# Kernel tuning notes

Measured on AMD Instinct MI355X. Metric: run time of the kernel, lower is better.

Reference implementation:

```python
import jax, jax.numpy as jnp
import numpy as np

EPS = 1e-5
N, K, C = 32768, 27, 128


def setup_inputs() -> dict:
    key = jax.random.key(0)
    k1, k2, k3, k4 = jax.random.split(key, 4)
    feats = jax.random.normal(k1, (N, C), dtype=jnp.float32)
    # Precomputed kernel-offset neighbor map (MinkowskiEngine kernel map),
    # one input index per (point, kernel offset).
    neighbors = jax.random.randint(k2, (N, K), 0, N, dtype=jnp.int32)
    scale = 1.0 / np.sqrt(K * C)  # fan-in init like sparse conv
    W1 = jax.random.normal(k3, (K, C, C), dtype=jnp.float32) * scale
    W2 = jax.random.normal(k4, (K, C, C), dtype=jnp.float32) * scale
    g1 = jnp.ones((C,), jnp.float32)
    b1 = jnp.zeros((C,), jnp.float32)
    g2 = jnp.ones((C,), jnp.float32)
    b2 = jnp.zeros((C,), jnp.float32)
    return {"feats": feats, "neighbors": neighbors, "W1": W1, "g1": g1,
            "b1": b1, "W2": W2, "g2": g2, "b2": b2}


def _sparse_conv(f, nbr, W):
    # gather-GEMM-scatter: gather neighbor features per kernel offset,
    # contract with that offset's weight, sum over offsets.
    gathered = f[nbr]                      # [N, K, C]
    return jnp.einsum('nkc,kcd->nd', gathered, W)  # [N, C]


def _batch_norm(x, gamma, beta):
    mu = jnp.mean(x, axis=0)
    var = jnp.mean(jnp.square(x - mu), axis=0)
    return (x - mu) * jax.lax.rsqrt(var + EPS) * gamma + beta


def reference(feats, neighbors, W1, g1, b1, W2, g2, b2):
    out = _sparse_conv(feats, neighbors, W1)
    out = jax.nn.relu(_batch_norm(out, g1, b1))
    out = _sparse_conv(out, neighbors, W2)
    out = _batch_norm(out, g2, b2)
    return jax.nn.relu(out + feats)
```

## Files before the change

### kernel.cpp

```cpp
#include <hip/hip_runtime.h>
#include <stdint.h>

#define NPTS 32768
#define KOFF 27
#define CH   128
#define NC   (NPTS*CH)
#define KSPLIT 3
#define KPG  9
#define TILE_M 128
#define NITER (KPG*2)

typedef __attribute__((ext_vector_type(8))) short short8;
typedef __attribute__((ext_vector_type(4))) float f32x4;
typedef unsigned short u16;

__device__ __forceinline__ float bf2f(u16 u) {
    union { uint32_t i; float f; } v; v.i = ((uint32_t)u) << 16; return v.f;
}
__device__ __forceinline__ u16 f2bf(float f) {
    union { float f; uint32_t i; } v; v.f = f;
    return (u16)((v.i + 0x7FFF + ((v.i >> 16) & 1)) >> 16);
}

#define GLDS16(gp, lp) __builtin_amdgcn_global_load_lds( \
    (__attribute__((address_space(1))) void*)(gp),           \
    (__attribute__((address_space(3))) void*)(lp), 16, 0, 0)

__global__ __launch_bounds__(256)
void prep_kernel(const float* __restrict__ W1, const float* __restrict__ W2,
                 u16* __restrict__ W1t, u16* __restrict__ W2t,
                 const float* __restrict__ feats, u16* __restrict__ xbuf,
                 float* __restrict__ stat)
{
    __shared__ u16 t[128*129];
    const int b = blockIdx.x, tid = threadIdx.x;
    if (b < 2*KOFF) {
        if (b == 0) for (int i = tid; i < 512; i += 256) stat[i] = 0.0f;
        const float* src = (b < KOFF) ? W1 + (size_t)b*CH*CH : W2 + (size_t)(b-KOFF)*CH*CH;
        u16* dst         = (b < KOFF) ? W1t + (size_t)b*CH*CH : W2t + (size_t)(b-KOFF)*CH*CH;
        for (int e = tid; e < CH*CH; e += 256) {
            int c = e >> 7, d = e & 127;
            t[d*129 + c] = f2bf(src[e]);
        }
        __syncthreads();
        for (int e = tid; e < CH*CH; e += 256) {
            int d = e >> 7, c = e & 127;
            dst[e] = t[d*129 + c];
        }
    } else {
        size_t e = ((size_t)(b - 2*KOFF) * 256 + tid) * 8;
        float4 a = *(const float4*)(feats + e);
        float4 c = *(const float4*)(feats + e + 4);
        ushort4 lo, hi;
        lo.x = f2bf(a.x); lo.y = f2bf(a.y); lo.z = f2bf(a.z); lo.w = f2bf(a.w);
        hi.x = f2bf(c.x); hi.y = f2bf(c.y); hi.z = f2bf(c.z); hi.w = f2bf(c.w);
        *(ushort4*)(xbuf + e) = lo;
        *(ushort4*)(xbuf + e + 4) = hi;
    }
}

__global__ __launch_bounds__(256, 3)
void ResidualBlock_77498389889548_kernel(const u16* __restrict__ xb,
                                         const int* __restrict__ nbr,
                                         const u16* __restrict__ Wt,
                                         u16* __restrict__ part)
{
    __shared__ __align__(16) u16 A_lds[TILE_M*64];
    __shared__ __align__(16) u16 B_lds[CH*64];
    __shared__ int idx_lds[KPG*TILE_M];

    const int tid = threadIdx.x;
    const int n0  = blockIdx.x * TILE_M;
    const int kg  = blockIdx.y;

    for (int e = tid; e < KPG*TILE_M; e += 256) {
        int kk = e >> 7, r = e & 127;
        int nb = nbr[(size_t)(n0 + r)*KOFF + kg*KPG + kk];
        idx_lds[e] = ((unsigned)nb < (unsigned)NPTS) ? nb : 0;
    }
    __syncthreads();

    const int wave = tid >> 6;
    const int lane = tid & 63;
    const int wrow = (wave >> 1) * 64;
    const int wcol = (wave & 1) * 64;
    const int lm   = lane & 15;
    const int quad = lane >> 4;
    const int l8r  = lane >> 3;
    const int swz  = ((lane & 7) ^ l8r) << 3;

    f32x4 acc[4][4];
    #pragma unroll
    for (int i = 0; i < 4; ++i)
        #pragma unroll
        for (int j = 0; j < 4; ++j)
            #pragma unroll
            for (int r = 0; r < 4; ++r) acc[i][j][r] = 0.0f;

    int aoff[2][4], boff[2][4];
    #pragma unroll
    for (int kc = 0; kc < 2; ++kc) {
        int g = kc*4 + quad;
        #pragma unroll
        for (int i = 0; i < 4; ++i) {
            int row = wrow + i*16 + lm;
            aoff[kc][i] = row*128 + ((g ^ (row & 7)) << 4);
        }
        #pragma unroll
        for (int j = 0; j < 4; ++j) {
            int d = wcol + j*16 + lm;
            boff[kc][j] = d*128 + ((g ^ (d & 7)) << 4);
        }
    }

    const char* Ab = (const char*)A_lds;
    const char* Bb = (const char*)B_lds;

    for (int it = 0; it < NITER; ++it) {
        const int h  = (it >= KPG) ? 1 : 0;
        const int kk = it - h*KPG;

        const u16* wb = Wt + (size_t)(kg*KPG + kk)*CH*CH + h*64 + swz;
        #pragma unroll
        for (int j = 0; j < 4; ++j) {
            int row8 = wave*32 + j*8;
            GLDS16(wb + (size_t)(row8 + l8r)*CH, &B_lds[row8*64]);
        }
        int nb4[4];
        #pragma unroll
        for (int j = 0; j < 4; ++j)
            nb4[j] = idx_lds[kk*128 + wave*32 + j*8 + l8r];
        #pragma unroll
        for (int j = 0; j < 4; ++j) {
            int row8 = wave*32 + j*8;
            GLDS16(xb + (size_t)nb4[j]*CH + h*64 + swz, &A_lds[row8*64]);
        }
        __syncthreads();

        #pragma unroll
        for (int kc = 0; kc < 2; ++kc) {
            short8 a[4], b[4];
            #pragma unroll
            for (int i = 0; i < 4; ++i) a[i] = *(const short8*)(Ab + aoff[kc][i]);
            #pragma unroll
            for (int j = 0; j < 4; ++j) b[j] = *(const short8*)(Bb + boff[kc][j]);
            #pragma unroll
            for (int i = 0; i < 4; ++i)
                #pragma unroll
                for (int j = 0; j < 4; ++j)
                    acc[i][j] = __builtin_amdgcn_mfma_f32_16x16x32_bf16(a[i], b[j], acc[i][j], 0, 0, 0);
        }
        __syncthreads();
    }

    u16* pb = part + (size_t)kg * NC;
    const int colb = wcol + lm;
    #pragma unroll
    for (int i = 0; i < 4; ++i) {
        #pragma unroll
        for (int r = 0; r < 4; ++r) {
            int row = n0 + wrow + i*16 + quad*4 + r;
            u16* pp = pb + (size_t)row*CH + colb;
            #pragma unroll
            for (int j = 0; j < 4; ++j) pp[j*16] = f2bf(acc[i][j][r]);
        }
    }
}

__global__ __launch_bounds__(256)
void sumstats_kernel(const u16* __restrict__ p0, const u16* __restrict__ p1,
                     const u16* __restrict__ p2, u16* __restrict__ y,
                     float* __restrict__ gsum, float* __restrict__ gsq)
{
    __shared__ float ls[CH], lq[CH];
    const int tid = threadIdx.x;
    const int c8 = (tid & 15) * 8;
    const int r0 = tid >> 4;
    const int b = blockIdx.x;
    if (tid < CH) { ls[tid] = 0.0f; lq[tid] = 0.0f; }
    __syncthreads();

    float s[8], q[8];
    #pragma unroll
    for (int i = 0; i < 8; ++i) { s[i] = 0.0f; q[i] = 0.0f; }

    for (int r = r0; r < 128; r += 16) {
        size_t e = (size_t)(b*128 + r)*CH + c8;
        ushort4 a0 = *(const ushort4*)(p0 + e), a1 = *(const ushort4*)(p0 + e + 4);
        ushort4 b0 = *(const ushort4*)(p1 + e), b1 = *(const ushort4*)(p1 + e + 4);
        ushort4 d0 = *(const ushort4*)(p2 + e), d1 = *(const ushort4*)(p2 + e + 4);
        float v[8];
        v[0] = bf2f(a0.x) + bf2f(b0.x) + bf2f(d0.x);
        v[1] = bf2f(a0.y) + bf2f(b0.y) + bf2f(d0.y);
        v[2] = bf2f(a0.z) + bf2f(b0.z) + bf2f(d0.z);
        v[3] = bf2f(a0.w) + bf2f(b0.w) + bf2f(d0.w);
        v[4] = bf2f(a1.x) + bf2f(b1.x) + bf2f(d1.x);
        v[5] = bf2f(a1.y) + bf2f(b1.y) + bf2f(d1.y);
        v[6] = bf2f(a1.z) + bf2f(b1.z) + bf2f(d1.z);
        v[7] = bf2f(a1.w) + bf2f(b1.w) + bf2f(d1.w);
        ushort4 o0, o1;
        o0.x = f2bf(v[0]); o0.y = f2bf(v[1]); o0.z = f2bf(v[2]); o0.w = f2bf(v[3]);
        o1.x = f2bf(v[4]); o1.y = f2bf(v[5]); o1.z = f2bf(v[6]); o1.w = f2bf(v[7]);
        *(ushort4*)(y + e) = o0;
        *(ushort4*)(y + e + 4) = o1;
        #pragma unroll
        for (int i = 0; i < 8; ++i) { s[i] += v[i]; q[i] += v[i]*v[i]; }
    }
    #pragma unroll
    for (int i = 0; i < 8; ++i) {
        atomicAdd(&ls[c8 + i], s[i]);
        atomicAdd(&lq[c8 + i], q[i]);
    }
    __syncthreads();
    if (tid < CH) {
        atomicAdd(&gsum[tid], ls[tid]);
        atomicAdd(&gsq[tid],  lq[tid]);
    }
}

__global__ __launch_bounds__(256)
void norm_relu_kernel(const u16* __restrict__ y, const float* __restrict__ sums,
                      const float* __restrict__ sumsq, const float* __restrict__ gam,
                      const float* __restrict__ bet, u16* __restrict__ xo)
{
    __shared__ float sc[128], sh[128];
    const int tid = threadIdx.x;
    if (tid < 128) {
        float mu  = sums[tid] * (1.0f/NPTS);
        float var = fmaxf(sumsq[tid] * (1.0f/NPTS) - mu*mu, 0.0f);
        float rs  = rsqrtf(var + 1e-5f);
        float s   = rs * gam[tid];
        sc[tid] = s; sh[tid] = bet[tid] - mu*s;
    }
    __syncthreads();
    size_t e = ((size_t)blockIdx.x*256 + tid) * 8;
    int c0 = (int)(e & 127);
    ushort4 lo = *(const ushort4*)(y + e);
    ushort4 hi = *(const ushort4*)(y + e + 4);
    ushort4 o0, o1;
    o0.x = f2bf(fmaxf(bf2f(lo.x)*sc[c0+0] + sh[c0+0], 0.0f));
    o0.y = f2bf(fmaxf(bf2f(lo.y)*sc[c0+1] + sh[c0+1], 0.0f));
    o0.z = f2bf(fmaxf(bf2f(lo.z)*sc[c0+2] + sh[c0+2], 0.0f));
    o0.w = f2bf(fmaxf(bf2f(lo.w)*sc[c0+3] + sh[c0+3], 0.0f));
    o1.x = f2bf(fmaxf(bf2f(hi.x)*sc[c0+4] + sh[c0+4], 0.0f));
    o1.y = f2bf(fmaxf(bf2f(hi.y)*sc[c0+5] + sh[c0+5], 0.0f));
    o1.z = f2bf(fmaxf(bf2f(hi.z)*sc[c0+6] + sh[c0+6], 0.0f));
    o1.w = f2bf(fmaxf(bf2f(hi.w)*sc[c0+7] + sh[c0+7], 0.0f));
    *(ushort4*)(xo + e) = o0;
    *(ushort4*)(xo + e + 4) = o1;
}

__global__ __launch_bounds__(256)
void final_kernel(const u16* __restrict__ y, const float* __restrict__ sums,
                  const float* __restrict__ sumsq, const float* __restrict__ gam,
                  const float* __restrict__ bet, const float* __restrict__ feats,
                  float* __restrict__ out)
{
    __shared__ float sc[128], sh[128];
    const int tid = threadIdx.x;
    if (tid < 128) {
        float mu  = sums[tid] * (1.0f/NPTS);
        float var = fmaxf(sumsq[tid] * (1.0f/NPTS) - mu*mu, 0.0f);
        float rs  = rsqrtf(var + 1e-5f);
        float s   = rs * gam[tid];
        sc[tid] = s; sh[tid] = bet[tid] - mu*s;
    }
    __syncthreads();
    size_t e = ((size_t)blockIdx.x*256 + tid) * 4;
    int c0 = (int)(e & 127);
    ushort4 in = *(const ushort4*)(y + e);
    float4 ft = *(const float4*)(feats + e);
    float4 o;
    o.x = fmaxf(bf2f(in.x)*sc[c0+0] + sh[c0+0] + ft.x, 0.0f);
    o.y = fmaxf(bf2f(in.y)*sc[c0+1] + sh[c0+1] + ft.y, 0.0f);
    o.z = fmaxf(bf2f(in.z)*sc[c0+2] + sh[c0+2] + ft.z, 0.0f);
    o.w = fmaxf(bf2f(in.w)*sc[c0+3] + sh[c0+3] + ft.w, 0.0f);
    *(float4*)(out + e) = o;
}

extern "C" void kernel_launch(void* const* d_in, const int* in_sizes, int n_in,
                              void* d_out, int out_size, void* d_ws, size_t ws_size,
                              hipStream_t stream)
{
    const float* feats = (const float*)d_in[0];
    const int*   nbr   = (const int*)d_in[1];
    const float* W1    = (const float*)d_in[2];
    const float* g1    = (const float*)d_in[3];
    const float* b1    = (const float*)d_in[4];
    const float* W2    = (const float*)d_in[5];
    const float* g2    = (const float*)d_in[6];
    const float* b2    = (const float*)d_in[7];
    float* out = (float*)d_out;

    char* ws = (char*)d_ws;
    u16*   xbuf = (u16*)ws;
    u16*   prt  = xbuf + (size_t)NC;
    u16*   ybuf = prt + (size_t)3*NC;
    u16*   W1t  = ybuf + (size_t)NC;
    u16*   W2t  = W1t + (size_t)KOFF*CH*CH;
    float* stat = (float*)(W2t + (size_t)KOFF*CH*CH);

    prep_kernel<<<dim3(2*KOFF + NC/2048), 256, 0, stream>>>(W1, W2, W1t, W2t, feats, xbuf, stat);

    ResidualBlock_77498389889548_kernel<<<dim3(NPTS/TILE_M, KSPLIT), 256, 0, stream>>>(
        xbuf, nbr, W1t, prt);
    sumstats_kernel<<<dim3(NPTS/128), 256, 0, stream>>>(
        prt, prt + (size_t)NC, prt + (size_t)2*NC, ybuf, stat, stat + 128);
    norm_relu_kernel<<<dim3(NC/2048), 256, 0, stream>>>(ybuf, stat, stat + 128, g1, b1, xbuf);

    ResidualBlock_77498389889548_kernel<<<dim3(NPTS/TILE_M, KSPLIT), 256, 0, stream>>>(
        xbuf, nbr, W2t, prt);
    sumstats_kernel<<<dim3(NPTS/128), 256, 0, stream>>>(
        prt, prt + (size_t)NC, prt + (size_t)2*NC, ybuf, stat + 256, stat + 384);
    final_kernel<<<dim3(NC/1024), 256, 0, stream>>>(ybuf, stat + 256, stat + 384, g2, b2, feats, out);
}
```

Before: 197.1 us.

## Drop K-split, double-buffer LDS tiles, fuse batch-norm stats into conv epilogue

The conv kernel now handles all 27 kernel offsets per 128-row tile instead of splitting them across three blocks. This removes the three bf16 partial buffers and the separate sumstats pass. The gather/weight loads go through double-buffered LDS, so the next stage's global-to-LDS copy overlaps the current MFMA work. The epilogue writes bf16 outputs directly and accumulates per-channel sum and sum-of-squares into global stats via atomics. The grid shrinks to 256 blocks with launch bounds of 1 block per CU and twice the LDS, which reduces occupancy and parallelism. Statistics are now computed from fp32 accumulators rather than from rounded partial sums.

```diff
diff --git a/kernel.cpp b/kernel.cpp
--- a/kernel.cpp
+++ b/kernel.cpp
@@ -5,10 +5,8 @@
 #define KOFF 27
 #define CH   128
 #define NC   (NPTS*CH)
-#define KSPLIT 3
-#define KPG  9
 #define TILE_M 128
-#define NITER (KPG*2)
+#define NITER (KOFF*2)
 
 typedef __attribute__((ext_vector_type(8))) short short8;
 typedef __attribute__((ext_vector_type(4))) float f32x4;
@@ -59,25 +57,28 @@
     }
 }
 
-__global__ __launch_bounds__(256, 3)
+__global__ __launch_bounds__(256, 1)
 void ResidualBlock_77498389889548_kernel(const u16* __restrict__ xb,
                                          const int* __restrict__ nbr,
                                          const u16* __restrict__ Wt,
-                                         u16* __restrict__ part)
-{
-    __shared__ __align__(16) u16 A_lds[TILE_M*64];
-    __shared__ __align__(16) u16 B_lds[CH*64];
-    __shared__ int idx_lds[KPG*TILE_M];
+                                         u16* __restrict__ y,
+                                         float* __restrict__ gsum,
+                                         float* __restrict__ gsq)
+{
+    __shared__ __align__(16) u16 A_lds[2][TILE_M*64];
+    __shared__ __align__(16) u16 B_lds[2][CH*64];
+    __shared__ int idx_lds[KOFF*TILE_M];
+    __shared__ float ls[CH], lq[CH];
 
     const int tid = threadIdx.x;
     const int n0  = blockIdx.x * TILE_M;
-    const int kg  = blockIdx.y;
-
-    for (int e = tid; e < KPG*TILE_M; e += 256) {
-        int kk = e >> 7, r = e & 127;
-        int nb = nbr[(size_t)(n0 + r)*KOFF + kg*KPG + kk];
-        idx_lds[e] = ((unsigned)nb < (unsigned)NPTS) ? nb : 0;
-    }
+
+    const int* nbl = nbr + (size_t)n0 * KOFF;
+    for (int e = tid; e < KOFF*TILE_M; e += 256) {
+        int v = nbl[e];
+        idx_lds[e] = ((unsigned)v < (unsigned)NPTS) ? v : 0;
+    }
+    if (tid < CH) { ls[tid] = 0.0f; lq[tid] = 0.0f; }
     __syncthreads();
 
     const int wave = tid >> 6;
@@ -113,30 +114,37 @@
         }
     }
 
-    const char* Ab = (const char*)A_lds;
-    const char* Bb = (const char*)B_lds;
-
+    #define STAGE(buf, it)                                                     \
+    {                                                                          \
+        const int h_  = ((it) >= KOFF) ? 1 : 0;                                \
+        const int kk_ = (it) - h_*KOFF;                                        \
+        const u16* wb_ = Wt + (size_t)kk_*CH*CH + h_*64 + swz;                 \
+        _Pragma("unroll")                                                      \
+        for (int j_ = 0; j_ < 4; ++j_) {                                       \
+            int row8_ = wave*32 + j_*8;                                        \
+            GLDS16(wb_ + (size_t)(row8_ + l8r)*CH, &B_lds[buf][row8_*64]);     \
+        }                                                                      \
+        int nb4_[4];                                                           \
+        _Pragma("unroll")                                                      \
+        for (int j_ = 0; j_ < 4; ++j_)                                         \
+            nb4_[j_] = idx_lds[(wave*32 + j_*8 + l8r)*KOFF + kk_];             \
+        _Pragma("unroll")                                                      \
+        for (int j_ = 0; j_ < 4; ++j_) {                                       \
+            int row8_ = wave*32 + j_*8;                                        \
+            GLDS16(xb + (size_t)nb4_[j_]*CH + h_*64 + swz,                     \
+                   &A_lds[buf][row8_*64]);                                     \
+        }                                                                      \
+    }
+
+    STAGE(0, 0);
+    __syncthreads();
+
+    int cur = 0;
     for (int it = 0; it < NITER; ++it) {
-        const int h  = (it >= KPG) ? 1 : 0;
-        const int kk = it - h*KPG;
-
-        const u16* wb = Wt + (size_t)(kg*KPG + kk)*CH*CH + h*64 + swz;
-        #pragma unroll
-        for (int j = 0; j < 4; ++j) {
-            int row8 = wave*32 + j*8;
-            GLDS16(wb + (size_t)(row8 + l8r)*CH, &B_lds[row8*64]);
-        }
-        int nb4[4];
-        #pragma unroll
-        for (int j = 0; j < 4; ++j)
-            nb4[j] = idx_lds[kk*128 + wave*32 + j*8 + l8r];
-        #pragma unroll
-        for (int j = 0; j < 4; ++j) {
-            int row8 = wave*32 + j*8;
-            GLDS16(xb + (size_t)nb4[j]*CH + h*64 + swz, &A_lds[row8*64]);
-        }
-        __syncthreads();
-
+        if (it + 1 < NITER) STAGE(cur ^ 1, it + 1);
+
+        const char* Ab = (const char*)A_lds[cur];
+        const char* Bb = (const char*)B_lds[cur];
         #pragma unroll
         for (int kc = 0; kc < 2; ++kc) {
             short8 a[4], b[4];
@@ -151,65 +159,31 @@
                     acc[i][j] = __builtin_amdgcn_mfma_f32_16x16x32_bf16(a[i], b[j], acc[i][j], 0, 0, 0);
         }
         __syncthreads();
-    }
-
-    u16* pb = part + (size_t)kg * NC;
-    const int colb = wcol + lm;
+        cur ^= 1;
+    }
+    #undef STAGE
+
+    float s[4], q[4];
+    #pragma unroll
+    for (int j = 0; j < 4; ++j) { s[j] = 0.0f; q[j] = 0.0f; }
     #pragma unroll
     for (int i = 0; i < 4; ++i) {
         #pragma unroll
         for (int r = 0; r < 4; ++r) {
             int row = n0 + wrow + i*16 + quad*4 + r;
-            u16* pp = pb + (size_t)row*CH + colb;
-            #pragma unroll
-            for (int j = 0; j < 4; ++j) pp[j*16] = f2bf(acc[i][j][r]);
-        }
-    }
-}
-
-__global__ __launch_bounds__(256)
-void sumstats_kernel(const u16* __restrict__ p0, const u16* __restrict__ p1,
-                     const u16* __restrict__ p2, u16* __restrict__ y,
-                     float* __restrict__ gsum, float* __restrict__ gsq)
-{
-    __shared__ float ls[CH], lq[CH];
-    const int tid = threadIdx.x;
-    const int c8 = (tid & 15) * 8;
-    const int r0 = tid >> 4;
-    const int b = blockIdx.x;
-    if (tid < CH) { ls[tid] = 0.0f; lq[tid] = 0.0f; }
-    __syncthreads();
-
-    float s[8], q[8];
-    #pragma unroll
-    for (int i = 0; i < 8; ++i) { s[i] = 0.0f; q[i] = 0.0f; }
-
-    for (int r = r0; r < 128; r += 16) {
-        size_t e = (size_t)(b*128 + r)*CH + c8;
-        ushort4 a0 = *(const ushort4*)(p0 + e), a1 = *(const ushort4*)(p0 + e + 4);
-        ushort4 b0 = *(const ushort4*)(p1 + e), b1 = *(const ushort4*)(p1 + e + 4);
-        ushort4 d0 = *(const ushort4*)(p2 + e), d1 = *(const ushort4*)(p2 + e + 4);
-        float v[8];
-        v[0] = bf2f(a0.x) + bf2f(b0.x) + bf2f(d0.x);
-        v[1] = bf2f(a0.y) + bf2f(b0.y) + bf2f(d0.y);
-        v[2] = bf2f(a0.z) + bf2f(b0.z) + bf2f(d0.z);
-        v[3] = bf2f(a0.w) + bf2f(b0.w) + bf2f(d0.w);
-        v[4] = bf2f(a1.x) + bf2f(b1.x) + bf2f(d1.x);
-        v[5] = bf2f(a1.y) + bf2f(b1.y) + bf2f(d1.y);
-        v[6] = bf2f(a1.z) + bf2f(b1.z) + bf2f(d1.z);
-        v[7] = bf2f(a1.w) + bf2f(b1.w) + bf2f(d1.w);
-        ushort4 o0, o1;
-        o0.x = f2bf(v[0]); o0.y = f2bf(v[1]); o0.z = f2bf(v[2]); o0.w = f2bf(v[3]);
-        o1.x = f2bf(v[4]); o1.y = f2bf(v[5]); o1.z = f2bf(v[6]); o1.w = f2bf(v[7]);
-        *(ushort4*)(y + e) = o0;
-        *(ushort4*)(y + e + 4) = o1;
-        #pragma unroll
-        for (int i = 0; i < 8; ++i) { s[i] += v[i]; q[i] += v[i]*v[i]; }
-    }
-    #pragma unroll
-    for (int i = 0; i < 8; ++i) {
-        atomicAdd(&ls[c8 + i], s[i]);
-        atomicAdd(&lq[c8 + i], q[i]);
+            u16* pp = y + (size_t)row*CH + wcol + lm;
+            #pragma unroll
+            for (int j = 0; j < 4; ++j) {
+                float v = acc[i][j][r];
+                pp[j*16] = f2bf(v);
+                s[j] += v; q[j] += v*v;
+            }
+        }
+    }
+    #pragma unroll
+    for (int j = 0; j < 4; ++j) {
+        atomicAdd(&ls[wcol + j*16 + lm], s[j]);
+        atomicAdd(&lq[wcol + j*16 + lm], q[j]);
     }
     __syncthreads();
     if (tid < CH) {
@@ -294,23 +268,18 @@
 
     char* ws = (char*)d_ws;
     u16*   xbuf = (u16*)ws;
-    u16*   prt  = xbuf + (size_t)NC;
-    u16*   ybuf = prt + (size_t)3*NC;
+    u16*   ybuf = xbuf + (size_t)NC;
     u16*   W1t  = ybuf + (size_t)NC;
     u16*   W2t  = W1t + (size_t)KOFF*CH*CH;
     float* stat = (float*)(W2t + (size_t)KOFF*CH*CH);
 
     prep_kernel<<<dim3(2*KOFF + NC/2048), 256, 0, stream>>>(W1, W2, W1t, W2t, feats, xbuf, stat);
 
-    ResidualBlock_77498389889548_kernel<<<dim3(NPTS/TILE_M, KSPLIT), 256, 0, stream>>>(
-        xbuf, nbr, W1t, prt);
-    sumstats_kernel<<<dim3(NPTS/128), 256, 0, stream>>>(
-        prt, prt + (size_t)NC, prt + (size_t)2*NC, ybuf, stat, stat + 128);
+    ResidualBlock_77498389889548_kernel<<<dim3(NPTS/TILE_M), 256, 0, stream>>>(
+        xbuf, nbr, W1t, ybuf, stat, stat + 128);
     norm_relu_kernel<<<dim3(NC/2048), 256, 0, stream>>>(ybuf, stat, stat + 128, g1, b1, xbuf);
 
-    ResidualBlock_77498389889548_kernel<<<dim3(NPTS/TILE_M, KSPLIT), 256, 0, stream>>>(
-        xbuf, nbr, W2t, prt);
-    sumstats_kernel<<<dim3(NPTS/128), 256, 0, stream>>>(
-        prt, prt + (size_t)NC, prt + (size_t)2*NC, ybuf, stat + 256, stat + 384);
+    ResidualBlock_77498389889548_kernel<<<dim3(NPTS/TILE_M), 256, 0, stream>>>(
+        xbuf, nbr, W2t, ybuf, stat + 256, stat + 384);
     final_kernel<<<dim3(NC/1024), 256, 0, stream>>>(ybuf, stat + 256, stat + 384, g2, b2, feats, out);
 }
```

Result: slower. 275.4 us (+39.7%).

## Fuse split-K reduction and BN stats into conv kernel via last-block counter

Applied to the files above, without the earlier changes.

Removes the separate sumstats kernel by having the last of the three K-split blocks for each row tile (detected with a per-tile atomic counter and threadfences) sum the bf16 partials, write y, and accumulate BN sums. This saves two kernel launches and lets the reduction overlap with other GEMM blocks still running. The cost is extra shared memory, a fence and an atomic in every block, plus counters that are zeroed only once per call by prep.

```diff
diff --git a/kernel.cpp b/kernel.cpp
--- a/kernel.cpp
+++ b/kernel.cpp
@@ -35,7 +35,7 @@
     __shared__ u16 t[128*129];
     const int b = blockIdx.x, tid = threadIdx.x;
     if (b < 2*KOFF) {
-        if (b == 0) for (int i = tid; i < 512; i += 256) stat[i] = 0.0f;
+        if (b == 0) for (int i = tid; i < 1024; i += 256) stat[i] = 0.0f;
         const float* src = (b < KOFF) ? W1 + (size_t)b*CH*CH : W2 + (size_t)(b-KOFF)*CH*CH;
         u16* dst         = (b < KOFF) ? W1t + (size_t)b*CH*CH : W2t + (size_t)(b-KOFF)*CH*CH;
         for (int e = tid; e < CH*CH; e += 256) {
@@ -63,11 +63,17 @@
 void ResidualBlock_77498389889548_kernel(const u16* __restrict__ xb,
                                          const int* __restrict__ nbr,
                                          const u16* __restrict__ Wt,
-                                         u16* __restrict__ part)
+                                         u16* __restrict__ part,
+                                         u16* __restrict__ y,
+                                         float* __restrict__ gsum,
+                                         float* __restrict__ gsq,
+                                         int* __restrict__ cnt)
 {
     __shared__ __align__(16) u16 A_lds[TILE_M*64];
     __shared__ __align__(16) u16 B_lds[CH*64];
     __shared__ int idx_lds[KPG*TILE_M];
+    __shared__ float ls[CH], lq[CH];
+    __shared__ int s_old;
 
     const int tid = threadIdx.x;
     const int n0  = blockIdx.x * TILE_M;
@@ -165,56 +171,57 @@
             for (int j = 0; j < 4; ++j) pp[j*16] = f2bf(acc[i][j][r]);
         }
     }
-}
-
-__global__ __launch_bounds__(256)
-void sumstats_kernel(const u16* __restrict__ p0, const u16* __restrict__ p1,
-                     const u16* __restrict__ p2, u16* __restrict__ y,
-                     float* __restrict__ gsum, float* __restrict__ gsq)
-{
-    __shared__ float ls[CH], lq[CH];
-    const int tid = threadIdx.x;
-    const int c8 = (tid & 15) * 8;
-    const int r0 = tid >> 4;
-    const int b = blockIdx.x;
-    if (tid < CH) { ls[tid] = 0.0f; lq[tid] = 0.0f; }
-    __syncthreads();
-
-    float s[8], q[8];
-    #pragma unroll
-    for (int i = 0; i < 8; ++i) { s[i] = 0.0f; q[i] = 0.0f; }
-
-    for (int r = r0; r < 128; r += 16) {
-        size_t e = (size_t)(b*128 + r)*CH + c8;
-        ushort4 a0 = *(const ushort4*)(p0 + e), a1 = *(const ushort4*)(p0 + e + 4);
-        ushort4 b0 = *(const ushort4*)(p1 + e), b1 = *(const ushort4*)(p1 + e + 4);
-        ushort4 d0 = *(const ushort4*)(p2 + e), d1 = *(const ushort4*)(p2 + e + 4);
-        float v[8];
-        v[0] = bf2f(a0.x) + bf2f(b0.x) + bf2f(d0.x);
-        v[1] = bf2f(a0.y) + bf2f(b0.y) + bf2f(d0.y);
-        v[2] = bf2f(a0.z) + bf2f(b0.z) + bf2f(d0.z);
-        v[3] = bf2f(a0.w) + bf2f(b0.w) + bf2f(d0.w);
-        v[4] = bf2f(a1.x) + bf2f(b1.x) + bf2f(d1.x);
-        v[5] = bf2f(a1.y) + bf2f(b1.y) + bf2f(d1.y);
-        v[6] = bf2f(a1.z) + bf2f(b1.z) + bf2f(d1.z);
-        v[7] = bf2f(a1.w) + bf2f(b1.w) + bf2f(d1.w);
-        ushort4 o0, o1;
-        o0.x = f2bf(v[0]); o0.y = f2bf(v[1]); o0.z = f2bf(v[2]); o0.w = f2bf(v[3]);
-        o1.x = f2bf(v[4]); o1.y = f2bf(v[5]); o1.z = f2bf(v[6]); o1.w = f2bf(v[7]);
-        *(ushort4*)(y + e) = o0;
-        *(ushort4*)(y + e + 4) = o1;
-        #pragma unroll
-        for (int i = 0; i < 8; ++i) { s[i] += v[i]; q[i] += v[i]*v[i]; }
-    }
-    #pragma unroll
-    for (int i = 0; i < 8; ++i) {
-        atomicAdd(&ls[c8 + i], s[i]);
-        atomicAdd(&lq[c8 + i], q[i]);
-    }
-    __syncthreads();
-    if (tid < CH) {
-        atomicAdd(&gsum[tid], ls[tid]);
-        atomicAdd(&gsq[tid],  lq[tid]);
+
+    __threadfence();
+    __syncthreads();
+    if (tid == 0) s_old = atomicAdd(&cnt[blockIdx.x], 1);
+    __syncthreads();
+    if (s_old == 2) {
+        __threadfence();
+        if (tid < CH) { ls[tid] = 0.0f; lq[tid] = 0.0f; }
+        __syncthreads();
+
+        const u16* p0 = part;
+        const u16* p1 = part + (size_t)NC;
+        const u16* p2 = part + (size_t)2*NC;
+        const int c8 = (tid & 15) * 8;
+        const int r0 = tid >> 4;
+        float s[8], q[8];
+        #pragma unroll
+        for (int i = 0; i < 8; ++i) { s[i] = 0.0f; q[i] = 0.0f; }
+
+        for (int r = r0; r < TILE_M; r += 16) {
+            size_t e = (size_t)(n0 + r)*CH + c8;
+            ushort4 a0 = *(const ushort4*)(p0 + e), a1 = *(const ushort4*)(p0 + e + 4);
+            ushort4 b0 = *(const ushort4*)(p1 + e), b1 = *(const ushort4*)(p1 + e + 4);
+            ushort4 d0 = *(const ushort4*)(p2 + e), d1 = *(const ushort4*)(p2 + e + 4);
+            float v[8];
+            v[0] = bf2f(a0.x) + bf2f(b0.x) + bf2f(d0.x);
+            v[1] = bf2f(a0.y) + bf2f(b0.y) + bf2f(d0.y);
+            v[2] = bf2f(a0.z) + bf2f(b0.z) + bf2f(d0.z);
+            v[3] = bf2f(a0.w) + bf2f(b0.w) + bf2f(d0.w);
+            v[4] = bf2f(a1.x) + bf2f(b1.x) + bf2f(d1.x);
+            v[5] = bf2f(a1.y) + bf2f(b1.y) + bf2f(d1.y);
+            v[6] = bf2f(a1.z) + bf2f(b1.z) + bf2f(d1.z);
+            v[7] = bf2f(a1.w) + bf2f(b1.w) + bf2f(d1.w);
+            ushort4 o0, o1;
+            o0.x = f2bf(v[0]); o0.y = f2bf(v[1]); o0.z = f2bf(v[2]); o0.w = f2bf(v[3]);
+            o1.x = f2bf(v[4]); o1.y = f2bf(v[5]); o1.z = f2bf(v[6]); o1.w = f2bf(v[7]);
+            *(ushort4*)(y + e) = o0;
+            *(ushort4*)(y + e + 4) = o1;
+            #pragma unroll
+            for (int i = 0; i < 8; ++i) { s[i] += v[i]; q[i] += v[i]*v[i]; }
+        }
+        #pragma unroll
+        for (int i = 0; i < 8; ++i) {
+            atomicAdd(&ls[c8 + i], s[i]);
+            atomicAdd(&lq[c8 + i], q[i]);
+        }
+        __syncthreads();
+        if (tid < CH) {
+            atomicAdd(&gsum[tid], ls[tid]);
+            atomicAdd(&gsq[tid],  lq[tid]);
+        }
     }
 }
 
@@ -299,18 +306,15 @@
     u16*   W1t  = ybuf + (size_t)NC;
     u16*   W2t  = W1t + (size_t)KOFF*CH*CH;
     float* stat = (float*)(W2t + (size_t)KOFF*CH*CH);
+    int*   cnt  = (int*)(stat + 512);
 
     prep_kernel<<<dim3(2*KOFF + NC/2048), 256, 0, stream>>>(W1, W2, W1t, W2t, feats, xbuf, stat);
 
     ResidualBlock_77498389889548_kernel<<<dim3(NPTS/TILE_M, KSPLIT), 256, 0, stream>>>(
-        xbuf, nbr, W1t, prt);
-    sumstats_kernel<<<dim3(NPTS/128), 256, 0, stream>>>(
-        prt, prt + (size_t)NC, prt + (size_t)2*NC, ybuf, stat, stat + 128);
+        xbuf, nbr, W1t, prt, ybuf, stat, stat + 128, cnt);
     norm_relu_kernel<<<dim3(NC/2048), 256, 0, stream>>>(ybuf, stat, stat + 128, g1, b1, xbuf);
 
     ResidualBlock_77498389889548_kernel<<<dim3(NPTS/TILE_M, KSPLIT), 256, 0, stream>>>(
-        xbuf, nbr, W2t, prt);
-    sumstats_kernel<<<dim3(NPTS/128), 256, 0, stream>>>(
-        prt, prt + (size_t)NC, prt + (size_t)2*NC, ybuf, stat + 256, stat + 384);
+        xbuf, nbr, W2t, prt, ybuf, stat + 256, stat + 384, cnt + 256);
     final_kernel<<<dim3(NC/1024), 256, 0, stream>>>(ybuf, stat + 256, stat + 384, g2, b2, feats, out);
 }
```

Result: slower. 445.6 us (+126.1%).

## Fuse BN stats and normalize via in-kernel grid barrier, keeping sums in registers

Applied to the files above, without the earlier changes.

Merges the partial-sum/statistics kernel with the normalize+ReLU (and final residual) kernel. Each block keeps its 128x128 tile of summed values in registers across a software grid barrier (atomic counter plus flag spin). This removes the intermediate bf16 y buffer write and read and one launch per BN. The barrier relies on all 256 blocks being co-resident and adds spin-wait latency. The counters are zeroed in the prep kernel.

```diff
diff --git a/kernel.cpp b/kernel.cpp
--- a/kernel.cpp
+++ b/kernel.cpp
@@ -35,7 +35,7 @@
     __shared__ u16 t[128*129];
     const int b = blockIdx.x, tid = threadIdx.x;
     if (b < 2*KOFF) {
-        if (b == 0) for (int i = tid; i < 512; i += 256) stat[i] = 0.0f;
+        if (b == 0) for (int i = tid; i < 1024; i += 256) stat[i] = 0.0f;
         const float* src = (b < KOFF) ? W1 + (size_t)b*CH*CH : W2 + (size_t)(b-KOFF)*CH*CH;
         u16* dst         = (b < KOFF) ? W1t + (size_t)b*CH*CH : W2t + (size_t)(b-KOFF)*CH*CH;
         for (int e = tid; e < CH*CH; e += 256) {
@@ -167,44 +167,60 @@
     }
 }
 
+__device__ __forceinline__ void grid_barrier(int* cnt, int nblk)
+{
+    __threadfence();
+    __syncthreads();
+    if (threadIdx.x == 0) {
+        int* flag = cnt + 1;
+        int old = atomicAdd(cnt, 1);
+        if (old == nblk - 1) {
+            __hip_atomic_store(flag, 1, __ATOMIC_RELEASE, __HIP_MEMORY_SCOPE_AGENT);
+        } else {
+            while (!__hip_atomic_load(flag, __ATOMIC_ACQUIRE, __HIP_MEMORY_SCOPE_AGENT))
+                __builtin_amdgcn_s_sleep(32);
+        }
+    }
+    __syncthreads();
+    __threadfence();
+}
+
 __global__ __launch_bounds__(256)
-void sumstats_kernel(const u16* __restrict__ p0, const u16* __restrict__ p1,
-                     const u16* __restrict__ p2, u16* __restrict__ y,
-                     float* __restrict__ gsum, float* __restrict__ gsq)
-{
-    __shared__ float ls[CH], lq[CH];
+void sumnorm_kernel(const u16* __restrict__ p0, const u16* __restrict__ p1,
+                    const u16* __restrict__ p2,
+                    const float* __restrict__ gam, const float* __restrict__ bet,
+                    float* __restrict__ gsum, float* __restrict__ gsq,
+                    int* __restrict__ cnt, u16* __restrict__ xo)
+{
+    __shared__ float ls[CH], lq[CH], sc[CH], sh[CH];
     const int tid = threadIdx.x;
-    const int c8 = (tid & 15) * 8;
-    const int r0 = tid >> 4;
-    const int b = blockIdx.x;
+    const int b   = blockIdx.x;
+    const int c8  = (tid & 15) * 8;
+    const int r0  = tid >> 4;
     if (tid < CH) { ls[tid] = 0.0f; lq[tid] = 0.0f; }
     __syncthreads();
 
+    float y[8][8];
     float s[8], q[8];
     #pragma unroll
     for (int i = 0; i < 8; ++i) { s[i] = 0.0f; q[i] = 0.0f; }
 
-    for (int r = r0; r < 128; r += 16) {
-        size_t e = (size_t)(b*128 + r)*CH + c8;
+    #pragma unroll
+    for (int k = 0; k < 8; ++k) {
+        size_t e = (size_t)(b*128 + r0 + k*16)*CH + c8;
         ushort4 a0 = *(const ushort4*)(p0 + e), a1 = *(const ushort4*)(p0 + e + 4);
         ushort4 b0 = *(const ushort4*)(p1 + e), b1 = *(const ushort4*)(p1 + e + 4);
         ushort4 d0 = *(const ushort4*)(p2 + e), d1 = *(const ushort4*)(p2 + e + 4);
-        float v[8];
-        v[0] = bf2f(a0.x) + bf2f(b0.x) + bf2f(d0.x);
-        v[1] = bf2f(a0.y) + bf2f(b0.y) + bf2f(d0.y);
-        v[2] = bf2f(a0.z) + bf2f(b0.z) + bf2f(d0.z);
-        v[3] = bf2f(a0.w) + bf2f(b0.w) + bf2f(d0.w);
-        v[4] = bf2f(a1.x) + bf2f(b1.x) + bf2f(d1.x);
-        v[5] = bf2f(a1.y) + bf2f(b1.y) + bf2f(d1.y);
-        v[6] = bf2f(a1.z) + bf2f(b1.z) + bf2f(d1.z);
-        v[7] = bf2f(a1.w) + bf2f(b1.w) + bf2f(d1.w);
-        ushort4 o0, o1;
-        o0.x = f2bf(v[0]); o0.y = f2bf(v[1]); o0.z = f2bf(v[2]); o0.w = f2bf(v[3]);
-        o1.x = f2bf(v[4]); o1.y = f2bf(v[5]); o1.z = f2bf(v[6]); o1.w = f2bf(v[7]);
-        *(ushort4*)(y + e) = o0;
-        *(ushort4*)(y + e + 4) = o1;
-        #pragma unroll
-        for (int i = 0; i < 8; ++i) { s[i] += v[i]; q[i] += v[i]*v[i]; }
+        y[k][0] = bf2f(a0.x) + bf2f(b0.x) + bf2f(d0.x);
+        y[k][1] = bf2f(a0.y) + bf2f(b0.y) + bf2f(d0.y);
+        y[k][2] = bf2f(a0.z) + bf2f(b0.z) + bf2f(d0.z);
+        y[k][3] = bf2f(a0.w) + bf2f(b0.w) + bf2f(d0.w);
+        y[k][4] = bf2f(a1.x) + bf2f(b1.x) + bf2f(d1.x);
+        y[k][5] = bf2f(a1.y) + bf2f(b1.y) + bf2f(d1.y);
+        y[k][6] = bf2f(a1.z) + bf2f(b1.z) + bf2f(d1.z);
+        y[k][7] = bf2f(a1.w) + bf2f(b1.w) + bf2f(d1.w);
+        #pragma unroll
+        for (int i = 0; i < 8; ++i) { s[i] += y[k][i]; q[i] += y[k][i]*y[k][i]; }
     }
     #pragma unroll
     for (int i = 0; i < 8; ++i) {
@@ -216,66 +232,112 @@
         atomicAdd(&gsum[tid], ls[tid]);
         atomicAdd(&gsq[tid],  lq[tid]);
     }
+
+    grid_barrier(cnt, gridDim.x);
+
+    if (tid < CH) {
+        float mu  = gsum[tid] * (1.0f/NPTS);
+        float var = fmaxf(gsq[tid] * (1.0f/NPTS) - mu*mu, 0.0f);
+        float rs  = rsqrtf(var + 1e-5f);
+        float scv = rs * gam[tid];
+        sc[tid] = scv; sh[tid] = bet[tid] - mu*scv;
+    }
+    __syncthreads();
+
+    #pragma unroll
+    for (int k = 0; k < 8; ++k) {
+        size_t e = (size_t)(b*128 + r0 + k*16)*CH + c8;
+        ushort4 o0, o1;
+        o0.x = f2bf(fmaxf(y[k][0]*sc[c8+0] + sh[c8+0], 0.0f));
+        o0.y = f2bf(fmaxf(y[k][1]*sc[c8+1] + sh[c8+1], 0.0f));
+        o0.z = f2bf(fmaxf(y[k][2]*sc[c8+2] + sh[c8+2], 0.0f));
+        o0.w = f2bf(fmaxf(y[k][3]*sc[c8+3] + sh[c8+3], 0.0f));
+        o1.x = f2bf(fmaxf(y[k][4]*sc[c8+4] + sh[c8+4], 0.0f));
+        o1.y = f2bf(fmaxf(y[k][5]*sc[c8+5] + sh[c8+5], 0.0f));
+        o1.z = f2bf(fmaxf(y[k][6]*sc[c8+6] + sh[c8+6], 0.0f));
+        o1.w = f2bf(fmaxf(y[k][7]*sc[c8+7] + sh[c8+7], 0.0f));
+        *(ushort4*)(xo + e) = o0;
+        *(ushort4*)(xo + e + 4) = o1;
+    }
 }
 
 __global__ __launch_bounds__(256)
-void norm_relu_kernel(const u16* __restrict__ y, const float* __restrict__ sums,
-                      const float* __restrict__ sumsq, const float* __restrict__ gam,
-                      const float* __restrict__ bet, u16* __restrict__ xo)
-{
-    __shared__ float sc[128], sh[128];
+void sumfinal_kernel(const u16* __restrict__ p0, const u16* __restrict__ p1,
+                     const u16* __restrict__ p2,
+                     const float* __restrict__ gam, const float* __restrict__ bet,
+                     float* __restrict__ gsum, float* __restrict__ gsq,
+                     int* __restrict__ cnt, const float* __restrict__ feats,
+                     float* __restrict__ out)
+{
+    __shared__ float ls[CH], lq[CH], sc[CH], sh[CH];
     const int tid = threadIdx.x;
-    if (tid < 128) {
-        float mu  = sums[tid] * (1.0f/NPTS);
-        float var = fmaxf(sumsq[tid] * (1.0f/NPTS) - mu*mu, 0.0f);
+    const int b   = blockIdx.x;
+    const int c8  = (tid & 15) * 8;
+    const int r0  = tid >> 4;
+    if (tid < CH) { ls[tid] = 0.0f; lq[tid] = 0.0f; }
+    __syncthreads();
+
+    float y[8][8];
+    float s[8], q[8];
+    #pragma unroll
+    for (int i = 0; i < 8; ++i) { s[i] = 0.0f; q[i] = 0.0f; }
+
+    #pragma unroll
+    for (int k = 0; k < 8; ++k) {
+        size_t e = (size_t)(b*128 + r0 + k*16)*CH + c8;
+        ushort4 a0 = *(const ushort4*)(p0 + e), a1 = *(const ushort4*)(p0 + e + 4);
+        ushort4 b0 = *(const ushort4*)(p1 + e), b1 = *(const ushort4*)(p1 + e + 4);
+        ushort4 d0 = *(const ushort4*)(p2 + e), d1 = *(const ushort4*)(p2 + e + 4);
+        y[k][0] = bf2f(a0.x) + bf2f(b0.x) + bf2f(d0.x);
+        y[k][1] = bf2f(a0.y) + bf2f(b0.y) + bf2f(d0.y);
+        y[k][2] = bf2f(a0.z) + bf2f(b0.z) + bf2f(d0.z);
+        y[k][3] = bf2f(a0.w) + bf2f(b0.w) + bf2f(d0.w);
+        y[k][4] = bf2f(a1.x) + bf2f(b1.x) + bf2f(d1.x);
+        y[k][5] = bf2f(a1.y) + bf2f(b1.y) + bf2f(d1.y);
+        y[k][6] = bf2f(a1.z) + bf2f(b1.z) + bf2f(d1.z);
+        y[k][7] = bf2f(a1.w) + bf2f(b1.w) + bf2f(d1.w);
+        #pragma unroll
+        for (int i = 0; i < 8; ++i) { s[i] += y[k][i]; q[i] += y[k][i]*y[k][i]; }
+    }
+    #pragma unroll
+    for (int i = 0; i < 8; ++i) {
+        atomicAdd(&ls[c8 + i], s[i]);
+        atomicAdd(&lq[c8 + i], q[i]);
+    }
+    __syncthreads();
+    if (tid < CH) {
+        atomicAdd(&gsum[tid], ls[tid]);
+        atomicAdd(&gsq[tid],  lq[tid]);
+    }
+
+    grid_barrier(cnt, gridDim.x);
+
+    if (tid < CH) {
+        float mu  = gsum[tid] * (1.0f/NPTS);
+        float var = fmaxf(gsq[tid] * (1.0f/NPTS) - mu*mu, 0.0f);
         float rs  = rsqrtf(var + 1e-5f);
-        float s   = rs * gam[tid];
-        sc[tid] = s; sh[tid] = bet[tid] - mu*s;
-    }
-    __syncthreads();
-    size_t e = ((size_t)blockIdx.x*256 + tid) * 8;
-    int c0 = (int)(e & 127);
-    ushort4 lo = *(const ushort4*)(y + e);
-    ushort4 hi = *(const ushort4*)(y + e + 4);
-    ushort4 o0, o1;
-    o0.x = f2bf(fmaxf(bf2f(lo.x)*sc[c0+0] + sh[c0+0], 0.0f));
-    o0.y = f2bf(fmaxf(bf2f(lo.y)*sc[c0+1] + sh[c0+1], 0.0f));
-    o0.z = f2bf(fmaxf(bf2f(lo.z)*sc[c0+2] + sh[c0+2], 0.0f));
-    o0.w = f2bf(fmaxf(bf2f(lo.w)*sc[c0+3] + sh[c0+3], 0.0f));
-    o1.x = f2bf(fmaxf(bf2f(hi.x)*sc[c0+4] + sh[c0+4], 0.0f));
-    o1.y = f2bf(fmaxf(bf2f(hi.y)*sc[c0+5] + sh[c0+5], 0.0f));
-    o1.z = f2bf(fmaxf(bf2f(hi.z)*sc[c0+6] + sh[c0+6], 0.0f));
-    o1.w = f2bf(fmaxf(bf2f(hi.w)*sc[c0+7] + sh[c0+7], 0.0f));
-    *(ushort4*)(xo + e) = o0;
-    *(ushort4*)(xo + e + 4) = o1;
-}
-
-__global__ __launch_bounds__(256)
-void final_kernel(const u16* __restrict__ y, const float* __restrict__ sums,
-                  const float* __restrict__ sumsq, const float* __restrict__ gam,
-                  const float* __restrict__ bet, const float* __restrict__ feats,
-                  float* __restrict__ out)
-{
-    __shared__ float sc[128], sh[128];
-    const int tid = threadIdx.x;
-    if (tid < 128) {
-        float mu  = sums[tid] * (1.0f/NPTS);
-        float var = fmaxf(sumsq[tid] * (1.0f/NPTS) - mu*mu, 0.0f);
-        float rs  = rsqrtf(var + 1e-5f);
-        float s   = rs * gam[tid];
-        sc[tid] = s; sh[tid] = bet[tid] - mu*s;
-    }
-    __syncthreads();
-    size_t e = ((size_t)blockIdx.x*256 + tid) * 4;
-    int c0 = (int)(e & 127);
-    ushort4 in = *(const ushort4*)(y + e);
-    float4 ft = *(const float4*)(feats + e);
-    float4 o;
-    o.x = fmaxf(bf2f(in.x)*sc[c0+0] + sh[c0+0] + ft.x, 0.0f);
-    o.y = fmaxf(bf2f(in.y)*sc[c0+1] + sh[c0+1] + ft.y, 0.0f);
-    o.z = fmaxf(bf2f(in.z)*sc[c0+2] + sh[c0+2] + ft.z, 0.0f);
-    o.w = fmaxf(bf2f(in.w)*sc[c0+3] + sh[c0+3] + ft.w, 0.0f);
-    *(float4*)(out + e) = o;
+        float scv = rs * gam[tid];
+        sc[tid] = scv; sh[tid] = bet[tid] - mu*scv;
+    }
+    __syncthreads();
+
+    #pragma unroll
+    for (int k = 0; k < 8; ++k) {
+        size_t e = (size_t)(b*128 + r0 + k*16)*CH + c8;
+        float4 f0 = *(const float4*)(feats + e);
+        float4 f1 = *(const float4*)(feats + e + 4);
+        float4 o0, o1;
+        o0.x = fmaxf(y[k][0]*sc[c8+0] + sh[c8+0] + f0.x, 0.0f);
+        o0.y = fmaxf(y[k][1]*sc[c8+1] + sh[c8+1] + f0.y, 0.0f);
+        o0.z = fmaxf(y[k][2]*sc[c8+2] + sh[c8+2] + f0.z, 0.0f);
+        o0.w = fmaxf(y[k][3]*sc[c8+3] + sh[c8+3] + f0.w, 0.0f);
+        o1.x = fmaxf(y[k][4]*sc[c8+4] + sh[c8+4] + f1.x, 0.0f);
+        o1.y = fmaxf(y[k][5]*sc[c8+5] + sh[c8+5] + f1.y, 0.0f);
+        o1.z = fmaxf(y[k][6]*sc[c8+6] + sh[c8+6] + f1.z, 0.0f);
+        o1.w = fmaxf(y[k][7]*sc[c8+7] + sh[c8+7] + f1.w, 0.0f);
+        *(float4*)(out + e) = o0;
+        *(float4*)(out + e + 4) = o1;
+    }
 }
 
 extern "C" void kernel_launch(void* const* d_in, const int* in_sizes, int n_in,
@@ -295,22 +357,21 @@
     char* ws = (char*)d_ws;
     u16*   xbuf = (u16*)ws;
     u16*   prt  = xbuf + (size_t)NC;
-    u16*   ybuf = prt + (size_t)3*NC;
-    u16*   W1t  = ybuf + (size_t)NC;
+    u16*   W1t  = prt + (size_t)3*NC;
     u16*   W2t  = W1t + (size_t)KOFF*CH*CH;
     float* stat = (float*)(W2t + (size_t)KOFF*CH*CH);
+    int*   cnt1 = (int*)(stat + 512);
+    int*   cnt2 = (int*)(stat + 516);
 
     prep_kernel<<<dim3(2*KOFF + NC/2048), 256, 0, stream>>>(W1, W2, W1t, W2t, feats, xbuf, stat);
 
     ResidualBlock_77498389889548_kernel<<<dim3(NPTS/TILE_M, KSPLIT), 256, 0, stream>>>(
         xbuf, nbr, W1t, prt);
-    sumstats_kernel<<<dim3(NPTS/128), 256, 0, stream>>>(
-        prt, prt + (size_t)NC, prt + (size_t)2*NC, ybuf, stat, stat + 128);
-    norm_relu_kernel<<<dim3(NC/2048), 256, 0, stream>>>(ybuf, stat, stat + 128, g1, b1, xbuf);
+    sumnorm_kernel<<<dim3(NPTS/128), 256, 0, stream>>>(
+        prt, prt + (size_t)NC, prt + (size_t)2*NC, g1, b1, stat, stat + 128, cnt1, xbuf);
 
     ResidualBlock_77498389889548_kernel<<<dim3(NPTS/TILE_M, KSPLIT), 256, 0, stream>>>(
         xbuf, nbr, W2t, prt);
-    sumstats_kernel<<<dim3(NPTS/128), 256, 0, stream>>>(
-        prt, prt + (size_t)NC, prt + (size_t)2*NC, ybuf, stat + 256, stat + 384);
-    final_kernel<<<dim3(NC/1024), 256, 0, stream>>>(ybuf, stat + 256, stat + 384, g2, b2, feats, out);
-}
+    sumfinal_kernel<<<dim3(NPTS/128), 256, 0, stream>>>(
+        prt, prt + (size_t)NC, prt + (size_t)2*NC, g2, b2, stat + 256, stat + 384, cnt2, feats, out);
+}
```

Result: slower. 266.1 us (+35.0%).
